# Kernel tuning notes

Hardware: AMD Instinct MI355X
Metric: run time of the kernel (lower is better)

The kernel has to match this reference:

```python
import jax, jax.numpy as jnp
import numpy as np

C = 512; H = 64; W = 64; STRIDE = 16; NA = 9; IMG = 1024
PRE_NMS = 6000; POST_NMS = 300; NMS_T = 0.7; MIN_SIZE = 16.0
BBOX_CLIP = float(np.log(1000.0 / 16.0))  # standard dw/dh clamp for exp() safety


def _make_anchors():
    # 3 scales x 3 aspect ratios on a stride-16 grid -> (H*W*9, 4) xyxy anchors
    scales = np.array([128.0, 256.0, 512.0])
    ratios = np.array([0.5, 1.0, 2.0])
    hs = (scales[:, None] * np.sqrt(ratios)[None, :]).ravel()
    ws = (scales[:, None] / np.sqrt(ratios)[None, :]).ravel()
    yy, xx = np.meshgrid((np.arange(H) + 0.5) * STRIDE, (np.arange(W) + 0.5) * STRIDE, indexing='ij')
    ctr = np.stack([xx.ravel(), yy.ravel()], -1)            # (HW, 2) centers
    wh = np.stack([ws, hs], -1)                              # (9, 2)
    anc = np.concatenate([ctr[:, None, :] - 0.5 * wh[None], ctr[:, None, :] + 0.5 * wh[None]], -1)
    return anc.reshape(-1, 4).astype(np.float32)             # (HW*9, 4)


def setup_inputs() -> dict:
    key = jax.random.key(0)
    k = jax.random.split(key, 4)
    return {
        'feature_map': jax.random.normal(k[0], (1, C, H, W), jnp.float32),
        'anchors': jnp.asarray(_make_anchors()),
        'image_shape': jnp.array([IMG, IMG], jnp.int32),
        'conv1_w': 0.01 * jax.random.normal(k[1], (C, C, 3, 3), jnp.float32),
        'conv1_b': jnp.zeros((C,), jnp.float32),
        'cls_w': 0.01 * jax.random.normal(k[2], (NA, C, 1, 1), jnp.float32),
        'cls_b': jnp.zeros((NA,), jnp.float32),
        'box_w': 0.01 * jax.random.normal(k[3], (NA * 4, C, 1, 1), jnp.float32),
        'box_b': jnp.zeros((NA * 4,), jnp.float32),
    }


def _conv(x, w, b):
    dn = ('NCHW', 'OIHW', 'NCHW')
    return jax.lax.conv_general_dilated(x, w, (1, 1), 'SAME', dimension_numbers=dn) + b[None, :, None, None]


def _decode_boxes(deltas, anchors):
    aw = anchors[:, 2] - anchors[:, 0]
    ah = anchors[:, 3] - anchors[:, 1]
    ax = anchors[:, 0] + 0.5 * aw
    ay = anchors[:, 1] + 0.5 * ah
    dx, dy, dw, dh = deltas[:, 0], deltas[:, 1], deltas[:, 2], deltas[:, 3]
    dw = jnp.minimum(dw, BBOX_CLIP)
    dh = jnp.minimum(dh, BBOX_CLIP)
    px = dx * aw + ax
    py = dy * ah + ay
    pw = jnp.exp(dw) * aw
    ph = jnp.exp(dh) * ah
    return jnp.stack([px - 0.5 * pw, py - 0.5 * ph, px + 0.5 * pw, py + 0.5 * ph], -1)


def _pairwise_iou(a, b):
    area_a = (a[:, 2] - a[:, 0]) * (a[:, 3] - a[:, 1])
    area_b = (b[:, 2] - b[:, 0]) * (b[:, 3] - b[:, 1])
    lt = jnp.maximum(a[:, None, :2], b[None, :, :2])
    rb = jnp.minimum(a[:, None, 2:], b[None, :, 2:])
    wh = jnp.clip(rb - lt, 0.0)
    inter = wh[..., 0] * wh[..., 1]
    union = area_a[:, None] + area_b[None, :] - inter
    return jnp.where(union > 0, inter / union, 0.0)


def reference(feature_map, anchors, image_shape, conv1_w, conv1_b, cls_w, cls_b, box_w, box_b):
    # conv head
    y = jax.nn.relu(_conv(feature_map, conv1_w, conv1_b))
    scores = _conv(y, cls_w, cls_b).reshape(-1)            # (H*W*9,)  torch .view(-1) order
    deltas = _conv(y, box_w, box_b).reshape(-1, 4)         # (H*W*9, 4) torch .reshape(-1,4) order
    preds = _decode_boxes(deltas, anchors)

    # filter_proposals: sigmoid -> topk 6000 -> clamp -> min-size -> NMS(0.7) -> top 300
    s = jax.nn.sigmoid(scores)
    topv, topi = jax.lax.top_k(s, PRE_NMS)                  # sorted descending
    b = preds[topi]
    h_img = image_shape[0].astype(jnp.float32)
    w_img = image_shape[1].astype(jnp.float32)
    b = jnp.stack([jnp.clip(b[:, 0], 0.0, w_img), jnp.clip(b[:, 1], 0.0, h_img),
                   jnp.clip(b[:, 2], 0.0, w_img), jnp.clip(b[:, 3], 0.0, h_img)], -1)
    valid = ((b[:, 2] - b[:, 0]) >= MIN_SIZE) & ((b[:, 3] - b[:, 1]) >= MIN_SIZE)

    iou = _pairwise_iou(b, b)                               # (6000, 6000)
    idx = jnp.arange(PRE_NMS)

    def body(i, keep):  # greedy NMS in score order (boxes already sorted desc)
        sup = (iou[i] > NMS_T) & keep[i] & (idx > i)
        return keep & (~sup)

    keep = jax.lax.fori_loop(0, PRE_NMS, body, valid)
    fs = jnp.where(keep, topv, -1.0)                        # suppressed/invalid -> sentinel
    sc, i2 = jax.lax.top_k(fs, POST_NMS)
    return b[i2], sc
```

## Files before the change

### kernel.cpp

```cpp
#include <hip/hip_runtime.h>
#include <hip/hip_bf16.h>

typedef unsigned int u32;
typedef unsigned long long u64;
typedef float v2f __attribute__((ext_vector_type(2)));
typedef float v4f __attribute__((ext_vector_type(4)));

#define OFF_Y      0ull
#define OFF_WT     8388608ull
#define OFF_ZPART  8388608ull
#define OFF_SCORES 11337728ull
#define OFF_DRAW   11485184ull
#define OFF_HIST   12075008ull
#define OFF_TOPV   12665344ull
#define OFF_BOXES  12714496ull
#define OFF_VW     12812800ull
#define OFF_MASK   12813824ull

#define NS     36864
#define PRE    6000
#define POST   300
#define SORTN  8192
#define MROW   96
#define NBW    8

__global__ __launch_bounds__(256) void k_wtrans(const float* __restrict__ gw,
                                                float* __restrict__ wT) {
    int o = blockIdx.x * 256 + threadIdx.x;
    if (o >= 512 * 512 * 9) return;
    int ci = o / 4608;
    int r = o - ci * 4608;
    int k = r >> 9;
    int co = r & 511;
    wT[o] = gw[co * 4608 + ci * 9 + k];
}

#define CI 16
#define XROW 66
#define CHUNK_ELEMS (CI * 3 * XROW)
#define STAGE_IT 13
__global__ __launch_bounds__(256, 4) void k_conv1(const float* __restrict__ x,
                                                  const float* __restrict__ wT,
                                                  const float* __restrict__ gb,
                                                  float* __restrict__ y) {
    __shared__ float xs[CHUNK_ELEMS];
    const int t = threadIdx.x;
    const int tx = t & 63;
    const int wv = __builtin_amdgcn_readfirstlane(t >> 6);
    const int cob = (blockIdx.x & 15) << 5;
    const int h0 = blockIdx.x >> 4;
    const int co_base = cob + (wv << 3);

    int offs[STAGE_IT];
    u32 vmask = 0;
#pragma unroll
    for (int u = 0; u < STAGE_IT; ++u) {
        int idx = t + u * 256;
        offs[u] = 0;
        if (idx < CHUNK_ELEMS) {
            int ci = idx / (3 * XROW);
            int rem = idx - ci * (3 * XROW);
            int row = rem / XROW;
            int col = rem - row * XROW;
            int gr = h0 + row - 1, gc = col - 1;
            if ((unsigned)gr < 64u && (unsigned)gc < 64u) {
                offs[u] = ci * 4096 + (gr << 6) + gc;
                vmask |= 1u << u;
            }
        }
    }

    v2f acc2[4];
#pragma unroll
    for (int j = 0; j < 4; ++j) acc2[j] = (v2f){0.f, 0.f};

    float st[STAGE_IT];
#pragma unroll
    for (int u = 0; u < STAGE_IT; ++u)
        st[u] = (vmask >> u & 1) ? x[offs[u]] : 0.f;

#pragma unroll 1
    for (int cc = 0; cc < 32; ++cc) {
        if (cc) __syncthreads();
#pragma unroll
        for (int u = 0; u < STAGE_IT; ++u) {
            int idx = t + u * 256;
            if (idx < CHUNK_ELEMS) xs[idx] = st[u];
        }
        __syncthreads();
        if (cc + 1 < 32) {
            const float* xsrc = x + (cc + 1) * CI * 4096;
#pragma unroll
            for (int u = 0; u < STAGE_IT; ++u)
                st[u] = (vmask >> u & 1) ? xsrc[offs[u]] : 0.f;
        }

        const int cig0 = cc * CI;
#pragma unroll 2
        for (int ci = 0; ci < CI; ++ci) {
            float xr[9];
            {
                const float* xp = xs + ci * (3 * XROW) + tx;
#pragma unroll
                for (int r = 0; r < 3; ++r) {
                    xr[r * 3 + 0] = xp[r * XROW + 0];
                    xr[r * 3 + 1] = xp[r * XROW + 1];
                    xr[r * 3 + 2] = xp[r * XROW + 2];
                }
            }
            const v2f* wk2 = (const v2f*)(wT + (size_t)(cig0 + ci) * 4608 + co_base);
#pragma unroll
            for (int k = 0; k < 9; ++k) {
                v2f w0 = wk2[k * 256 + 0];
                v2f w1 = wk2[k * 256 + 1];
                v2f w2 = wk2[k * 256 + 2];
                v2f w3 = wk2[k * 256 + 3];
                float xv = xr[k];
                v2f xp2 = {xv, xv};
                acc2[0] = __builtin_elementwise_fma(w0, xp2, acc2[0]);
                acc2[1] = __builtin_elementwise_fma(w1, xp2, acc2[1]);
                acc2[2] = __builtin_elementwise_fma(w2, xp2, acc2[2]);
                acc2[3] = __builtin_elementwise_fma(w3, xp2, acc2[3]);
            }
        }
    }

#pragma unroll
    for (int j = 0; j < 4; ++j) {
        int co0 = co_base + 2 * j;
        float v0 = acc2[j].x + gb[co0];
        float v1 = acc2[j].y + gb[co0 + 1];
        v0 = v0 > 0.f ? v0 : 0.f;
        v1 = v1 > 0.f ? v1 : 0.f;
        y[co0 * 4096 + (h0 << 6) + tx] = v0;
        y[(co0 + 1) * 4096 + (h0 << 6) + tx] = v1;
    }
}

__global__ __launch_bounds__(256) void k_heads_part(const float* __restrict__ y,
                                                    const float* __restrict__ cw,
                                                    const float* __restrict__ bw,
                                                    float* __restrict__ zpart,
                                                    u32* __restrict__ hist) {
    __shared__ __align__(16) float ys[64][132];
    const int t = threadIdx.x;
    {
        int hb = blockIdx.x << 9;
        hist[hb + t] = 0u;
        hist[hb + 256 + t] = 0u;
    }
    const int px = t & 63;
    const int gu = __builtin_amdgcn_readfirstlane(t >> 6);
    const int px0 = (blockIdx.x & 63) << 6;
    const int q = blockIdx.x >> 6;
    const int cib = q << 7;
    const int nch = (gu == 0) ? 12 : 11;

    const float* wrow[12];
#pragma unroll
    for (int j = 0; j < 12; ++j) {
        int ch = gu + 4 * j;
        if (ch < 9) wrow[j] = cw + ch * 512;
        else if (ch < 45) wrow[j] = bw + (ch - 9) * 512;
        else wrow[j] = cw;
    }
    float acc[12];
#pragma unroll
    for (int j = 0; j < 12; ++j) acc[j] = 0.f;

    for (int idx = t; idx < 128 * 64; idx += 256) {
        int ci = idx >> 6;
        int pp = idx & 63;
        ys[pp][ci] = y[(cib + ci) * 4096 + px0 + pp];
    }
    __syncthreads();

#pragma unroll 1
    for (int cq = 0; cq < 32; ++cq) {
        float4 yv = *(const float4*)&ys[px][cq << 2];
        float4 wv[12];
#pragma unroll
        for (int j = 0; j < 12; ++j)
            if (j < nch) wv[j] = *(const float4*)(wrow[j] + cib + (cq << 2));
#pragma unroll
        for (int j = 0; j < 12; ++j)
            if (j < nch)
                acc[j] += wv[j].x * yv.x + wv[j].y * yv.y + wv[j].z * yv.z + wv[j].w * yv.w;
    }
    for (int j = 0; j < nch; ++j) {
        int ch = gu + 4 * j;
        zpart[((q * 45 + ch) << 12) + px0 + px] = acc[j];
    }
}

__global__ __launch_bounds__(256) void k_hreduce(const float* __restrict__ zpart,
                                                 const float* __restrict__ cb,
                                                 const float* __restrict__ bb,
                                                 float* __restrict__ scores,
                                                 float* __restrict__ draw,
                                                 u32* __restrict__ hist) {
    int i = blockIdx.x * 256 + threadIdx.x;
    if (i >= 45 * 4096) return;
    int ch = i >> 12;
    int sp = i & 4095;
    float z = zpart[((0 * 45 + ch) << 12) + sp] + zpart[((1 * 45 + ch) << 12) + sp] +
              zpart[((2 * 45 + ch) << 12) + sp] + zpart[((3 * 45 + ch) << 12) + sp];
    if (ch < 9) {
        z += cb[ch];
        float s = 1.f / (1.f + expf(-z));
        scores[(ch << 12) + sp] = s;
        u32 sb = __float_as_uint(s);
        atomicAdd(&hist[sb >> 13], 1u);
    } else {
        z += bb[ch - 9];
        draw[((ch - 9) << 12) + sp] = z;
    }
}

__global__ __launch_bounds__(1024) void k_select(const u32* __restrict__ hist,
                                                 const float* __restrict__ scores,
                                                 const float* __restrict__ draw,
                                                 const float* __restrict__ anchors,
                                                 const int* __restrict__ ishape,
                                                 float* __restrict__ boxes,
                                                 float* __restrict__ topv,
                                                 u64* __restrict__ vw) {
    __shared__ u32 csum[1024];
    __shared__ u32 suf[1024];
    __shared__ u64 sk[SORTN];
    __shared__ int sel_s, cnt_s;
    const int t = threadIdx.x;

    u32 s = 0;
    {
        const uint4* hp4 = (const uint4*)(hist + t * 128);
#pragma unroll 4
        for (int i = 0; i < 32; ++i) {
            uint4 h4 = hp4[i];
            s += h4.x + h4.y + h4.z + h4.w;
        }
    }
    csum[t] = s;
    suf[t] = s;
    if (t == 0) cnt_s = 0;
    __syncthreads();
    for (int off = 1; off < 1024; off <<= 1) {
        u32 v = suf[t] + ((t + off < 1024) ? suf[t + off] : 0u);
        __syncthreads();
        suf[t] = v;
        __syncthreads();
    }
    u32 above = suf[t] - csum[t];
    if (above < (u32)PRE && suf[t] >= (u32)PRE) {
        const u32* hp = hist + t * 128;
        u32 run = above;
        int bstar = t * 128;
        u32 found = 0;
        for (int b2 = 127; b2 >= 0; --b2) {
            u32 c = hp[b2];
            if (!found && run + c >= (u32)PRE) { bstar = t * 128 + b2; found = 1; }
            if (!found) run += c;
        }
        sel_s = bstar;
    }
    for (int i = t; i < SORTN; i += 1024) sk[i] = 0;
    __syncthreads();

    const int sel = sel_s;
#pragma unroll 1
    for (int u = 0; u < 9; ++u) {
        int g = t + (u << 10);
        float4 s4 = *(const float4*)(scores + (g << 2));
#pragma unroll
        for (int e = 0; e < 4; ++e) {
            u32 sb = __float_as_uint(((const float*)&s4)[e]);
            if ((int)(sb >> 13) >= sel) {
                int p = atomicAdd(&cnt_s, 1);
                if (p < SORTN) sk[p] = ((u64)sb << 32) | (u32)(~((g << 2) + e));
            }
        }
    }
    __syncthreads();

    const int base = t << 3;
    u64 a[8];
    {
#pragma unroll
        for (int u = 0; u < 8; ++u) a[u] = sk[base + u];
#pragma unroll
        for (int k = 2; k <= 8; k <<= 1) {
#pragma unroll
            for (int j = k >> 1; j > 0; j >>= 1) {
#pragma unroll
                for (int u = 0; u < 8; ++u) {
                    if ((u & j) == 0) {
                        int l = u | j;
                        bool up = (((base + u) & k) == 0);
                        u64 x0 = a[u], x1 = a[l];
                        if (up ? (x0 < x1) : (x0 > x1)) { a[u] = x1; a[l] = x0; }
                    }
                }
            }
        }
#pragma unroll
        for (int u = 0; u < 8; ++u) sk[base + u] = a[u];
        __syncthreads();
    }
    for (int k = 16; k <= SORTN; k <<= 1) {
        for (int j = k >> 1; j >= 8; j >>= 1) {
#pragma unroll
            for (int s2 = 0; s2 < 4; ++s2) {
                int pidx = t + (s2 << 10);
                int i = ((pidx & ~(j - 1)) << 1) | (pidx & (j - 1));
                int l = i | j;
                u64 x0 = sk[i], x1 = sk[l];
                bool up = ((i & k) == 0);
                if (up ? (x0 < x1) : (x0 > x1)) { sk[i] = x1; sk[l] = x0; }
            }
            __syncthreads();
        }
#pragma unroll
        for (int u = 0; u < 8; ++u) a[u] = sk[base + u];
        {
            bool up = ((base & k) == 0);
#pragma unroll
            for (int j = 4; j > 0; j >>= 1) {
#pragma unroll
                for (int u = 0; u < 8; ++u) {
                    if ((u & j) == 0) {
                        int l = u | j;
                        u64 x0 = a[u], x1 = a[l];
                        if (up ? (x0 < x1) : (x0 > x1)) { a[u] = x1; a[l] = x0; }
                    }
                }
            }
        }
#pragma unroll
        for (int u = 0; u < 8; ++u) sk[base + u] = a[u];
        __syncthreads();
    }

    const float wimg = (float)ishape[1], himg = (float)ishape[0];
#pragma unroll 1
    for (int s2 = 0; s2 < 6; ++s2) {
        int r = (s2 << 10) + t;
        bool valid = false;
        if (r < PRE) {
            u64 key = sk[r];
            u32 sb = (u32)(key >> 32);
            int i = (int)(~(u32)key);
            topv[r] = __uint_as_float(sb);
            int c = i >> 10;
            int t4 = i & 1023;
            float4 d4 = *(const float4*)(draw + c * 4096 + (t4 << 2));
            float4 a4 = *(const float4*)(anchors + i * 4);
            float aw = a4.z - a4.x, ah = a4.w - a4.y;
            float ax = a4.x + 0.5f * aw, ay = a4.y + 0.5f * ah;
            const float CLIPV = (float)4.135166556742356;
            float dw = fminf(d4.z, CLIPV);
            float dh = fminf(d4.w, CLIPV);
            float px = d4.x * aw + ax, py = d4.y * ah + ay;
            float pw = expf(dw) * aw, ph = expf(dh) * ah;
            float x1 = fminf(fmaxf(px - 0.5f * pw, 0.f), wimg);
            float y1 = fminf(fmaxf(py - 0.5f * ph, 0.f), himg);
            float x2 = fminf(fmaxf(px + 0.5f * pw, 0.f), wimg);
            float y2 = fminf(fmaxf(py + 0.5f * ph, 0.f), himg);
            valid = (x2 - x1 >= 16.f) && (y2 - y1 >= 16.f);
            *(float4*)(boxes + r * 4) = make_float4(x1, y1, x2, y2);
        }
        u64 bm = __ballot(valid);
        if ((t & 63) == 0) vw[(s2 << 4) + (t >> 6)] = bm;
    }
}

__global__ __launch_bounds__(256) void k_mask(const float* __restrict__ boxes,
                                              u64* __restrict__ mask) {
    __shared__ float4 cbx[16 * 65];
    const int t = threadIdx.x;
    const int r0 = blockIdx.x << 4;
    const int row = r0 + (t >> 4);
    const int wloc = t & 15;
    float4 rb = *(const float4*)(boxes + row * 4);
    float area_a = (rb.z - rb.x) * (rb.w - rb.y);
    for (int chunk = 0; chunk < 6; ++chunk) {
        int j0c = chunk << 10;
        for (int idx = t; idx < 1024; idx += 256) {
            int j = j0c + idx;
            float4 v = make_float4(0.f, 0.f, 0.f, 0.f);
            if (j < PRE) v = *(const float4*)(boxes + j * 4);
            cbx[(idx >> 6) * 65 + (idx & 63)] = v;
        }
        __syncthreads();
        u64 bits = 0;
        const float4* cbr = cbx + wloc * 65;
        for (int b = 0; b < 64; ++b) {
            int j = j0c + (wloc << 6) + b;
            float4 ob = cbr[b];
            float area_b = (ob.z - ob.x) * (ob.w - ob.y);
            float ltx = fmaxf(rb.x, ob.x), lty = fmaxf(rb.y, ob.y);
            float rbx = fminf(rb.z, ob.z), rby = fminf(rb.w, ob.w);
            float wx = fmaxf(rbx - ltx, 0.f), wy = fmaxf(rby - lty, 0.f);
            float inter = wx * wy;
            float uni = area_a + area_b - inter;
            float iou = (uni > 0.f) ? (inter / uni) : 0.f;
            if (iou > 0.7f && j > row && j < PRE) bits |= (1ull << b);
        }
        mask[(size_t)row * MROW + (chunk << 4) + wloc] = bits;
        __syncthreads();
    }
}

__device__ __forceinline__ u64 shfl64(u64 v, int src) {
    u32 lo = __shfl((u32)v, src, 64);
    u32 hi = __shfl((u32)(v >> 32), src, 64);
    return ((u64)hi << 32) | lo;
}
__global__ __launch_bounds__(320) void k_nms_out(const u64* __restrict__ mask,
                                                 const u64* __restrict__ vw,
                                                 const float* __restrict__ boxes,
                                                 const float* __restrict__ topv,
                                                 float* __restrict__ out) {
    __shared__ u64 kws[MROW];
    __shared__ int keepl[POST];
    __shared__ int kc_s;
    const int tid = threadIdx.x;
    if (tid < MROW) kws[tid] = 0ull;
    __syncthreads();

    if (tid < 64) {
        const int lane = tid;
        u64 vw0 = (lane < 94) ? vw[lane] : 0ull;
        u64 vw1 = (lane < 30) ? vw[64 + lane] : 0ull;
        u64 rem0 = 0ull, rem1 = 0ull;
        int kc = 0;
        bool done = false;
        for (int w = 0; w < 94 && !done; ++w) {
            u64 vww  = (w < 64) ? shfl64(vw0, w)  : shfl64(vw1, w - 64);
            u64 remw = (w < 64) ? shfl64(rem0, w) : shfl64(rem1, w - 64);
            u64 aw = vww & ~remw;
            u64 kwbits = 0;
            while (aw && !done) {
                int bq[NBW];
                u64 tmp = aw;
#pragma unroll
                for (int q = 0; q < NBW; ++q) {
                    bq[q] = tmp ? __builtin_ctzll(tmp) : 64;
                    tmp &= tmp - 1;
                }
                u64 rq0[NBW], rq1[NBW];
#pragma unroll
                for (int q = 0; q < NBW; ++q) {
                    rq0[q] = 0ull; rq1[q] = 0ull;
                    if (bq[q] < 64) {
                        const u64* mrow = mask + (size_t)((w << 6) + bq[q]) * MROW;
                        rq0[q] = mrow[lane];
                        if (lane < 30) rq1[q] = mrow[64 + lane];
                    }
                }
#pragma unroll
                for (int q = 0; q < NBW; ++q) {
                    int b = bq[q];
                    if (b >= 64) break;
                    if (!((aw >> b) & 1ull)) continue;
                    if (lane == 0) keepl[kc] = (w << 6) + b;
                    kc++;
                    kwbits |= (1ull << b);
                    if (kc >= POST) { done = true; break; }
                    rem0 |= rq0[q];
                    rem1 |= rq1[q];
                    u64 roww = (w < 64) ? shfl64(rq0[q], w) : shfl64(rq1[q], w - 64);
                    aw &= ~roww;
                    aw &= ~(1ull << b);
                }
            }
            if (lane == 0) kws[w] = kwbits;
        }
        if (lane == 0) kc_s = kc;
    }
    __syncthreads();

    int j = tid;
    if (j >= POST) return;
    int kc2 = kc_s;
    int r;
    float sc;
    if (j < kc2) {
        r = keepl[j];
        sc = topv[r];
    } else {
        int target = j - kc2;
        r = PRE - 1;
        int cum = 0;
        for (int w = 0; w < 94; ++w) {
            u64 kb = kws[w];
            int nvalid = (w < 93) ? 64 : 48;
            u64 vmask2 = (nvalid == 64) ? ~0ull : ((1ull << nvalid) - 1ull);
            u64 nk = (~kb) & vmask2;
            int c = __popcll(nk);
            if (cum + c > target) {
                int need = target - cum;
                u64 m = nk;
                for (int q = 0; q < need; ++q) m &= (m - 1);
                r = (w << 6) + __builtin_ctzll(m);
                break;
            }
            cum += c;
        }
        sc = -1.0f;
    }
    out[j * 4 + 0] = boxes[r * 4 + 0];
    out[j * 4 + 1] = boxes[r * 4 + 1];
    out[j * 4 + 2] = boxes[r * 4 + 2];
    out[j * 4 + 3] = boxes[r * 4 + 3];
    out[1200 + j] = sc;
}

extern "C" void kernel_launch(void* const* d_in, const int* in_sizes, int n_in,
                              void* d_out, int out_size, void* d_ws, size_t ws_size,
                              hipStream_t stream) {
    const float* x = (const float*)d_in[0];
    const float* anchors = (const float*)d_in[1];
    const int* ishape = (const int*)d_in[2];
    const float* c1w = (const float*)d_in[3];
    const float* c1b = (const float*)d_in[4];
    const float* clw = (const float*)d_in[5];
    const float* clb = (const float*)d_in[6];
    const float* bxw = (const float*)d_in[7];
    const float* bxb = (const float*)d_in[8];

    char* ws = (char*)d_ws;
    float* y      = (float*)(ws + OFF_Y);
    float* wT     = (float*)(ws + OFF_WT);
    float* zpart  = (float*)(ws + OFF_ZPART);
    float* scores = (float*)(ws + OFF_SCORES);
    float* draw   = (float*)(ws + OFF_DRAW);
    u32*   hist   = (u32*)(ws + OFF_HIST);
    float* topv   = (float*)(ws + OFF_TOPV);
    float* boxes  = (float*)(ws + OFF_BOXES);
    u64*   vw     = (u64*)(ws + OFF_VW);
    u64*   mask   = (u64*)(ws + OFF_MASK);

    k_wtrans<<<(512 * 512 * 9 + 255) / 256, 256, 0, stream>>>(c1w, wT);
    k_conv1<<<1024, 256, 0, stream>>>(x, wT, c1b, y);
    k_heads_part<<<256, 256, 0, stream>>>(y, clw, bxw, zpart, hist);
    k_hreduce<<<(45 * 4096 + 255) / 256, 256, 0, stream>>>(zpart, clb, bxb, scores, draw, hist);
    k_select<<<1, 1024, 0, stream>>>(hist, scores, draw, anchors, ishape, boxes, topv, vw);
    k_mask<<<PRE / 16, 256, 0, stream>>>(boxes, mask);
    k_nms_out<<<1, 320, 0, stream>>>(mask, vw, boxes, topv, (float*)d_out);
}
```

Before: 672.8 us.

## Software-pipeline NMS mask row loads with double-buffered batches of candidates

```diff
diff --git a/kernel.cpp b/kernel.cpp
--- a/kernel.cpp
+++ b/kernel.cpp
@@ -22,7 +22,7 @@
 #define POST   300
 #define SORTN  8192
 #define MROW   96
-#define NBW    8
+#define NBW    16
 
 __global__ __launch_bounds__(256) void k_wtrans(const float* __restrict__ gw,
                                                 float* __restrict__ wT) {
@@ -438,39 +438,64 @@
             u64 vww  = (w < 64) ? shfl64(vw0, w)  : shfl64(vw1, w - 64);
             u64 remw = (w < 64) ? shfl64(rem0, w) : shfl64(rem1, w - 64);
             u64 aw = vww & ~remw;
+            if (!aw) continue;
             u64 kwbits = 0;
-            while (aw && !done) {
-                int bq[NBW];
-                u64 tmp = aw;
+            u64 pend = aw;
+            int bqA[NBW];
+            u64 ra0[NBW], ra1[NBW];
+#pragma unroll
+            for (int q = 0; q < NBW; ++q) {
+                bqA[q] = pend ? __builtin_ctzll(pend) : 64;
+                pend &= pend - 1;
+            }
+#pragma unroll
+            for (int q = 0; q < NBW; ++q) {
+                ra0[q] = 0ull; ra1[q] = 0ull;
+                if (bqA[q] < 64) {
+                    const u64* mrow = mask + (size_t)((w << 6) + bqA[q]) * MROW;
+                    ra0[q] = mrow[lane];
+                    if (lane < 30) ra1[q] = mrow[64 + lane];
+                }
+            }
+            for (;;) {
+                int bqB[NBW];
+                u64 rb0[NBW], rb1[NBW];
 #pragma unroll
                 for (int q = 0; q < NBW; ++q) {
-                    bq[q] = tmp ? __builtin_ctzll(tmp) : 64;
-                    tmp &= tmp - 1;
-                }
-                u64 rq0[NBW], rq1[NBW];
+                    bqB[q] = pend ? __builtin_ctzll(pend) : 64;
+                    pend &= pend - 1;
+                }
 #pragma unroll
                 for (int q = 0; q < NBW; ++q) {
-                    rq0[q] = 0ull; rq1[q] = 0ull;
-                    if (bq[q] < 64) {
-                        const u64* mrow = mask + (size_t)((w << 6) + bq[q]) * MROW;
-                        rq0[q] = mrow[lane];
-                        if (lane < 30) rq1[q] = mrow[64 + lane];
+                    rb0[q] = 0ull; rb1[q] = 0ull;
+                    if (bqB[q] < 64) {
+                        const u64* mrow = mask + (size_t)((w << 6) + bqB[q]) * MROW;
+                        rb0[q] = mrow[lane];
+                        if (lane < 30) rb1[q] = mrow[64 + lane];
                     }
                 }
 #pragma unroll
                 for (int q = 0; q < NBW; ++q) {
-                    int b = bq[q];
+                    int b = bqA[q];
                     if (b >= 64) break;
                     if (!((aw >> b) & 1ull)) continue;
                     if (lane == 0) keepl[kc] = (w << 6) + b;
                     kc++;
                     kwbits |= (1ull << b);
                     if (kc >= POST) { done = true; break; }
-                    rem0 |= rq0[q];
-                    rem1 |= rq1[q];
-                    u64 roww = (w < 64) ? shfl64(rq0[q], w) : shfl64(rq1[q], w - 64);
+                    rem0 |= ra0[q];
+                    rem1 |= ra1[q];
+                    u64 roww = (w < 64) ? shfl64(ra0[q], w) : shfl64(ra1[q], w - 64);
                     aw &= ~roww;
                     aw &= ~(1ull << b);
+                }
+                if (done) break;
+                if (bqB[0] >= 64) break;
+#pragma unroll
+                for (int q = 0; q < NBW; ++q) {
+                    bqA[q] = bqB[q];
+                    ra0[q] = rb0[q];
+                    ra1[q] = rb1[q];
                 }
             }
             if (lane == 0) kws[w] = kwbits;
```

New measurement: 676.9 us. No clear change (+0.6%).
